# Kernel tuning notes

Measured on AMD Instinct MI355X. Metric: run time of the kernel, lower is better.

Reference implementation:

```python
import jax, jax.numpy as jnp
import numpy as np

NEG_INF = -1e10  # matches torch -10000000000.0


def setup_inputs() -> dict:
    key = jax.random.key(0)
    ks = jax.random.split(key, 8)
    L, B, E, H, HID, A = 2048, 32, 512, 512, 512, 512
    input_data = jax.random.normal(ks[0], (L, B, E), dtype=jnp.float32)
    mask = jax.random.randint(ks[1], (L, B), 0, 2, dtype=jnp.int32)
    action_feature = jax.random.normal(ks[2], (B, A), dtype=jnp.float32)
    hidden_state = jax.random.normal(ks[3], (B, H), dtype=jnp.float32)
    state = jax.random.normal(ks[4], (B, H), dtype=jnp.float32)
    W1 = jax.random.normal(ks[5], (H + E, HID), dtype=jnp.float32) * (1.0 / np.sqrt(H + E))
    b1 = jnp.zeros((HID,), dtype=jnp.float32)
    W2 = jax.random.normal(ks[6], (HID, 1), dtype=jnp.float32) * (1.0 / np.sqrt(HID))
    b2 = jnp.zeros((1,), dtype=jnp.float32)
    return {"input_data": input_data, "mask": mask, "action_feature": action_feature,
            "hidden_state": hidden_state, "state": state,
            "W1": W1, "b1": b1, "W2": W2, "b2": b2}


def reference(input_data, mask, action_feature, hidden_state, state, W1, b1, W2, b2):
    # input_data: (L, B, E); hidden_state: (B, H)
    H = hidden_state.shape[-1]
    # query = concat([hidden broadcast over L, input_data], -1); split W1 to avoid
    # materializing the (L, B, H+E) concat.
    W1_h, W1_e = W1[:H], W1[H:]                      # (H, HID), (E, HID)
    pre = hidden_state @ W1_h + b1                   # (B, HID)
    pre = pre[None] + jnp.einsum('lbe,eh->lbh', input_data, W1_e)  # (L, B, HID)
    logit = (jnp.tanh(pre) @ W2).squeeze(-1) + b2[0]  # (L, B)
    logit = jnp.where(mask != 0, logit, NEG_INF)
    p = jax.nn.softmax(logit, axis=0)                 # softmax over L
    ctx = jnp.einsum('lbe,lb->be', input_data, p)     # (B, E)
    return jnp.concatenate([ctx, action_feature], axis=1)
```

## Files before the change

### kernel.cpp

```cpp
#include <hip/hip_runtime.h>
#include <hip/hip_bf16.h>
#include <stdint.h>

#define L_DIM 2048
#define B_DIM 32
#define E_DIM 512
#define HID_DIM 512
#define M_DIM (L_DIM * B_DIM)

typedef float f32x4 __attribute__((ext_vector_type(4)));
typedef short bf16x8 __attribute__((ext_vector_type(8)));

#define OFF_BASE  0
#define OFF_WT    65536
#define OFF_LOGIT 589824
#define OFF_P     851968
#define OFF_PART  1114112

__device__ __forceinline__ unsigned short f2bf(float f) {
  unsigned int u = __float_as_uint(f);
  u = (u + 0x7FFFu + ((u >> 16) & 1u)) >> 16;
  return (unsigned short)u;
}

__device__ __forceinline__ float tanh_fast(float x) {
  float xc = fminf(fmaxf(x, -15.f), 15.f);
  float e = __expf(2.f * xc);
  return (e - 1.f) * __builtin_amdgcn_rcpf(e + 1.f);
}

__device__ __forceinline__ uint4 pack8(const float4& a, const float4& b) {
  uint4 r;
  r.x = (unsigned)f2bf(a.x) | ((unsigned)f2bf(a.y) << 16);
  r.y = (unsigned)f2bf(a.z) | ((unsigned)f2bf(a.w) << 16);
  r.z = (unsigned)f2bf(b.x) | ((unsigned)f2bf(b.y) << 16);
  r.w = (unsigned)f2bf(b.z) | ((unsigned)f2bf(b.w) << 16);
  return r;
}

__global__ __launch_bounds__(256) void k_base(const float* __restrict__ hidden,
                                              const float* __restrict__ W1,
                                              const float* __restrict__ b1,
                                              float* __restrict__ base) {
  const int b = blockIdx.x;
  const int tid = threadIdx.x;
  __shared__ float hs[HID_DIM];
  {
    float2 v = *(const float2*)(hidden + (size_t)b * 512 + tid * 2);
    hs[tid * 2] = v.x; hs[tid * 2 + 1] = v.y;
  }
  __syncthreads();
  const int h = tid * 2;
  float2 b1v = *(const float2*)(b1 + h);
  float ax = b1v.x, ay = b1v.y;
#pragma unroll 8
  for (int e = 0; e < 512; ++e) {
    float2 w = *(const float2*)(W1 + (size_t)e * 512 + h);
    float hv = hs[e];
    ax = fmaf(hv, w.x, ax);
    ay = fmaf(hv, w.y, ay);
  }
  float2 r; r.x = ax; r.y = ay;
  *(float2*)(base + (size_t)b * 512 + h) = r;
}

__global__ __launch_bounds__(256) void k_prep_wt(const float* __restrict__ W1,
                                                 unsigned short* __restrict__ Wt) {
  const int kc = blockIdx.x;
  const int tid = threadIdx.x;
  __shared__ unsigned short sh[32][520];
#pragma unroll
  for (int i = 0; i < 16; ++i) {
    int flat4 = i * 256 + tid;
    int r = flat4 >> 7;
    int c = (flat4 & 127) * 4;
    float4 v = *(const float4*)(W1 + (size_t)(512 + kc * 32 + r) * 512 + c);
    sh[r][c + 0] = f2bf(v.x); sh[r][c + 1] = f2bf(v.y);
    sh[r][c + 2] = f2bf(v.z); sh[r][c + 3] = f2bf(v.w);
  }
  __syncthreads();
#pragma unroll
  for (int j = 0; j < 2; ++j) {
    int n = tid * 2 + j;
    alignas(16) unsigned short ov[32];
#pragma unroll
    for (int kl = 0; kl < 32; ++kl) ov[kl] = sh[kl][n];
    uint4* dst = (uint4*)(Wt + ((size_t)kc * 16384 + (size_t)n * 32));
    const uint4* s = (const uint4*)ov;
    dst[0] = s[0]; dst[1] = s[1]; dst[2] = s[2]; dst[3] = s[3];
  }
}

__global__ __launch_bounds__(512, 2) void k_logits(
    const float* __restrict__ x, const unsigned short* __restrict__ Wt,
    const float* __restrict__ base, const float* __restrict__ W2,
    float* __restrict__ logit) {
  __shared__ unsigned short xs[2][128 * 32];
  __shared__ unsigned short wl[2][512 * 32];
  const int tid = threadIdx.x;
  const int m0 = blockIdx.x * 128;
  const int wid = tid >> 6, lane = tid & 63;
  const int wm = wid >> 2, wn = wid & 3;
  const int lg = lane >> 4, l15 = lane & 15;

  const int xr = tid >> 2;
  const int xk = (tid & 3) * 8;
  const float* xsrc = x + (size_t)(m0 + xr) * 512 + xk;

  {
    float4 a0 = *(const float4*)(xsrc + 0);
    float4 a1 = *(const float4*)(xsrc + 4);
    const uint4* s = (const uint4*)(Wt + (size_t)tid * 32);
    uint4 w0 = s[0], w1 = s[1], w2_ = s[2], w3 = s[3];
    *(uint4*)(&xs[0][xr * 32 + xk]) = pack8(a0, a1);
    uint4* wd = (uint4*)(&wl[0][tid * 32]);
    wd[(0 + tid) & 3] = w0; wd[(1 + tid) & 3] = w1;
    wd[(2 + tid) & 3] = w2_; wd[(3 + tid) & 3] = w3;
  }
  __syncthreads();

  f32x4 acc[4][8];
#pragma unroll
  for (int mi = 0; mi < 4; ++mi)
#pragma unroll
    for (int ni = 0; ni < 8; ++ni) acc[mi][ni] = (f32x4){0.f, 0.f, 0.f, 0.f};

  for (int kc = 0; kc < 16; ++kc) {
    const int cur = kc & 1;
    float4 nxa, nxb; uint4 nw0, nw1, nw2, nw3;
    if (kc < 15) {
      nxa = *(const float4*)(xsrc + (kc + 1) * 32);
      nxb = *(const float4*)(xsrc + (kc + 1) * 32 + 4);
      const uint4* s = (const uint4*)(Wt + (size_t)(kc + 1) * 16384 + (size_t)tid * 32);
      nw0 = s[0]; nw1 = s[1]; nw2 = s[2]; nw3 = s[3];
    }
    bf16x8 af[4];
#pragma unroll
    for (int mi = 0; mi < 4; ++mi) {
      int r = wm * 64 + mi * 16 + l15;
      af[mi] = *(const bf16x8*)(&xs[cur][r * 32 + lg * 8]);
    }
    bf16x8 bf[8];
#pragma unroll
    for (int ni = 0; ni < 8; ++ni) {
      int n = wn * 128 + ni * 16 + l15;
      bf[ni] = *(const bf16x8*)(&wl[cur][n * 32 + ((lg + n) & 3) * 8]);
    }
#pragma unroll
    for (int mi = 0; mi < 4; ++mi)
#pragma unroll
      for (int ni = 0; ni < 8; ++ni)
        acc[mi][ni] = __builtin_amdgcn_mfma_f32_16x16x32_bf16(af[mi], bf[ni], acc[mi][ni], 0, 0, 0);
    if (kc < 15) {
      const int nb = cur ^ 1;
      *(uint4*)(&xs[nb][xr * 32 + xk]) = pack8(nxa, nxb);
      uint4* wd = (uint4*)(&wl[nb][tid * 32]);
      wd[(0 + tid) & 3] = nw0; wd[(1 + tid) & 3] = nw1;
      wd[(2 + tid) & 3] = nw2; wd[(3 + tid) & 3] = nw3;
    }
    __syncthreads();
  }

  float w2v[8];
#pragma unroll
  for (int ni = 0; ni < 8; ++ni) w2v[ni] = W2[wn * 128 + ni * 16 + l15];
  float lsum[4][4];
#pragma unroll
  for (int mi = 0; mi < 4; ++mi) {
#pragma unroll
    for (int rg = 0; rg < 4; ++rg) {
      int m = m0 + wm * 64 + mi * 16 + lg * 4 + rg;
      int bb = m & 31;
      const float* brow = base + (size_t)bb * 512 + wn * 128;
      float s = 0.f;
#pragma unroll
      for (int ni = 0; ni < 8; ++ni) {
        float pre = acc[mi][ni][rg] + brow[ni * 16 + l15];
        s = fmaf(tanh_fast(pre), w2v[ni], s);
      }
      lsum[mi][rg] = s;
    }
  }
  float (*lred)[4][64] = (float (*)[4][64])xs;
#pragma unroll
  for (int mi = 0; mi < 4; ++mi)
#pragma unroll
    for (int rg = 0; rg < 4; ++rg) {
      float v = lsum[mi][rg];
      v += __shfl_xor(v, 1); v += __shfl_xor(v, 2);
      v += __shfl_xor(v, 4); v += __shfl_xor(v, 8);
      if (l15 == 0) lred[wm][wn][mi * 16 + lg * 4 + rg] = v;
    }
  __syncthreads();
  if (tid < 128) {
    const int wmr = tid >> 6, row = tid & 63;
    float v = (lred[wmr][0][row] + lred[wmr][1][row]) +
              (lred[wmr][2][row] + lred[wmr][3][row]);
    logit[m0 + tid] = v;
  }
}

__global__ __launch_bounds__(256) void k_softmax(const float* __restrict__ logit,
                                                 const int* __restrict__ mask,
                                                 float* __restrict__ p) {
  const int b = blockIdx.x, tid = threadIdx.x;
  float lv[8]; float mx = -3.0e38f;
#pragma unroll
  for (int i = 0; i < 8; ++i) {
    int idx = (tid + i * 256) * 32 + b;
    float v = (mask[idx] != 0) ? logit[idx] : -1.0e10f;
    lv[i] = v; mx = fmaxf(mx, v);
  }
  __shared__ float red[8];
  for (int d = 1; d < 64; d <<= 1) mx = fmaxf(mx, __shfl_xor(mx, d));
  if ((tid & 63) == 0) red[tid >> 6] = mx;
  __syncthreads();
  mx = fmaxf(fmaxf(red[0], red[1]), fmaxf(red[2], red[3]));
  float s = 0.f;
#pragma unroll
  for (int i = 0; i < 8; ++i) { lv[i] = __expf(lv[i] - mx); s += lv[i]; }
  for (int d = 1; d < 64; d <<= 1) s += __shfl_xor(s, d);
  __syncthreads();
  if ((tid & 63) == 0) red[4 + (tid >> 6)] = s;
  __syncthreads();
  s = (red[4] + red[5]) + (red[6] + red[7]);
  float inv = 1.f / s;
#pragma unroll
  for (int i = 0; i < 8; ++i) {
    int idx = (tid + i * 256) * 32 + b;
    p[idx] = lv[i] * inv;
  }
}

__global__ __launch_bounds__(256) void k_ctx(const float* __restrict__ x,
                                             const float* __restrict__ p,
                                             float* __restrict__ part) {
  const int blk = blockIdx.x;
  const int b = blk >> 5, ch = blk & 31;
  const int tid = threadIdx.x;
  __shared__ float ps[64];
  const int l0 = ch * 64;
  if (tid < 64) ps[tid] = p[(l0 + tid) * 32 + b];
  __syncthreads();
  const float* xb = x + ((size_t)l0 * 32 + b) * 512 + tid * 2;
  float ax = 0.f, ay = 0.f;
#pragma unroll 4
  for (int i = 0; i < 64; ++i) {
    float2 v = *(const float2*)(xb + (size_t)i * 32 * 512);
    float pv = ps[i];
    ax = fmaf(pv, v.x, ax); ay = fmaf(pv, v.y, ay);
  }
  float2 r; r.x = ax; r.y = ay;
  *(float2*)(part + (size_t)blk * 512 + tid * 2) = r;
}

__global__ __launch_bounds__(256) void k_final(const float* __restrict__ part,
                                               const float* __restrict__ af,
                                               float* __restrict__ out) {
  const int b = blockIdx.x, tid = threadIdx.x;
  float ax = 0.f, ay = 0.f;
#pragma unroll
  for (int ch = 0; ch < 32; ++ch) {
    float2 v = *(const float2*)(part + ((size_t)(b * 32 + ch) * 512) + tid * 2);
    ax += v.x; ay += v.y;
  }
  float2 r; r.x = ax; r.y = ay;
  *(float2*)(out + (size_t)b * 1024 + tid * 2) = r;
  float2 a = *(const float2*)(af + (size_t)b * 512 + tid * 2);
  *(float2*)(out + (size_t)b * 1024 + 512 + tid * 2) = a;
}

extern "C" void kernel_launch(void* const* d_in, const int* in_sizes, int n_in,
                              void* d_out, int out_size, void* d_ws, size_t ws_size,
                              hipStream_t stream) {
  const float* x      = (const float*)d_in[0];
  const int*   mask   = (const int*)d_in[1];
  const float* af     = (const float*)d_in[2];
  const float* hidden = (const float*)d_in[3];
  const float* W1     = (const float*)d_in[5];
  const float* b1     = (const float*)d_in[6];
  const float* W2     = (const float*)d_in[7];
  float* out = (float*)d_out;
  char* ws = (char*)d_ws;
  float*          base  = (float*)(ws + OFF_BASE);
  unsigned short* Wt    = (unsigned short*)(ws + OFF_WT);
  float*          logit = (float*)(ws + OFF_LOGIT);
  float*          p     = (float*)(ws + OFF_P);
  float*          part  = (float*)(ws + OFF_PART);

  k_base   <<<32,   256, 0, stream>>>(hidden, W1, b1, base);
  k_prep_wt<<<16,   256, 0, stream>>>(W1, Wt);
  k_logits <<<512,  512, 0, stream>>>(x, Wt, base, W2, logit);
  k_softmax<<<32,   256, 0, stream>>>(logit, mask, p);
  k_ctx    <<<1024, 256, 0, stream>>>(x, p, part);
  k_final  <<<32,   256, 0, stream>>>(part, af, out);
}
```

Measured before the change: 123.3 us.

## Pre-swizzle W1 and x tiles into MFMA fragment order; widen ctx loads

The weight prep kernel now writes W1 in the exact per-lane fragment order the MFMA loop consumes. The x tile is also stored to shared memory in fragment order, so each lane reads its operand with one contiguous 16-byte LDS load and neither bank swizzling nor strided row access is needed. Global weight loads become fully coalesced uint4 reads across threads instead of 64-byte runs per thread. Separately, the ctx reduction uses float4 loads with 128 threads per block instead of float2 with 256.

New measurement: 118.5 us. -3.8%, faster.

```diff
diff --git a/kernel.cpp b/kernel.cpp
--- a/kernel.cpp
+++ b/kernel.cpp
@@ -68,26 +68,26 @@
                                                  unsigned short* __restrict__ Wt) {
   const int kc = blockIdx.x;
   const int tid = threadIdx.x;
-  __shared__ unsigned short sh[32][520];
+  __shared__ unsigned short sh[32][516];
 #pragma unroll
   for (int i = 0; i < 16; ++i) {
-    int flat4 = i * 256 + tid;
-    int r = flat4 >> 7;
-    int c = (flat4 & 127) * 4;
+    int f4 = i * 256 + tid;
+    int r = f4 >> 7;
+    int c = (f4 & 127) * 4;
     float4 v = *(const float4*)(W1 + (size_t)(512 + kc * 32 + r) * 512 + c);
     sh[r][c + 0] = f2bf(v.x); sh[r][c + 1] = f2bf(v.y);
     sh[r][c + 2] = f2bf(v.z); sh[r][c + 3] = f2bf(v.w);
   }
   __syncthreads();
 #pragma unroll
-  for (int j = 0; j < 2; ++j) {
-    int n = tid * 2 + j;
-    alignas(16) unsigned short ov[32];
-#pragma unroll
-    for (int kl = 0; kl < 32; ++kl) ov[kl] = sh[kl][n];
-    uint4* dst = (uint4*)(Wt + ((size_t)kc * 16384 + (size_t)n * 32));
-    const uint4* s = (const uint4*)ov;
-    dst[0] = s[0]; dst[1] = s[1]; dst[2] = s[2]; dst[3] = s[3];
+  for (int i = 0; i < 8; ++i) {
+    int u = i * 256 + tid;
+    int n = ((u >> 9) << 7) + (((u >> 6) & 7) << 4) + (u & 15);
+    int k0 = ((u >> 4) & 3) << 3;
+    alignas(16) unsigned short tmp[8];
+#pragma unroll
+    for (int j = 0; j < 8; ++j) tmp[j] = sh[k0 + j][n];
+    *(uint4*)(Wt + ((size_t)kc * 2048 + u) * 8) = *(const uint4*)tmp;
   }
 }
 
@@ -95,8 +95,8 @@
     const float* __restrict__ x, const unsigned short* __restrict__ Wt,
     const float* __restrict__ base, const float* __restrict__ W2,
     float* __restrict__ logit) {
-  __shared__ unsigned short xs[2][128 * 32];
-  __shared__ unsigned short wl[2][512 * 32];
+  __shared__ unsigned short xs[2][4096];
+  __shared__ unsigned short wl[2][16384];
   const int tid = threadIdx.x;
   const int m0 = blockIdx.x * 128;
   const int wid = tid >> 6, lane = tid & 63;
@@ -104,18 +104,20 @@
   const int lg = lane >> 4, l15 = lane & 15;
 
   const int xr = tid >> 2;
-  const int xk = (tid & 3) * 8;
-  const float* xsrc = x + (size_t)(m0 + xr) * 512 + xk;
+  const int xks = tid & 3;
+  const float* xsrc = x + (size_t)(m0 + xr) * 512 + xks * 8;
+  const int xu = ((xr >> 4) << 6) + (xks << 4) + (xr & 15);
 
   {
     float4 a0 = *(const float4*)(xsrc + 0);
     float4 a1 = *(const float4*)(xsrc + 4);
-    const uint4* s = (const uint4*)(Wt + (size_t)tid * 32);
-    uint4 w0 = s[0], w1 = s[1], w2_ = s[2], w3 = s[3];
-    *(uint4*)(&xs[0][xr * 32 + xk]) = pack8(a0, a1);
-    uint4* wd = (uint4*)(&wl[0][tid * 32]);
-    wd[(0 + tid) & 3] = w0; wd[(1 + tid) & 3] = w1;
-    wd[(2 + tid) & 3] = w2_; wd[(3 + tid) & 3] = w3;
+    *(uint4*)(&xs[0][xu * 8]) = pack8(a0, a1);
+    const uint4* s = (const uint4*)Wt;
+#pragma unroll
+    for (int j = 0; j < 4; ++j) {
+      uint4 w = s[j * 512 + tid];
+      *(uint4*)(&wl[0][(j * 512 + tid) * 8]) = w;
+    }
   }
   __syncthreads();
 
@@ -127,36 +129,33 @@
 
   for (int kc = 0; kc < 16; ++kc) {
     const int cur = kc & 1;
-    float4 nxa, nxb; uint4 nw0, nw1, nw2, nw3;
+    float4 nxa, nxb; uint4 nw[4];
     if (kc < 15) {
       nxa = *(const float4*)(xsrc + (kc + 1) * 32);
       nxb = *(const float4*)(xsrc + (kc + 1) * 32 + 4);
-      const uint4* s = (const uint4*)(Wt + (size_t)(kc + 1) * 16384 + (size_t)tid * 32);
-      nw0 = s[0]; nw1 = s[1]; nw2 = s[2]; nw3 = s[3];
+      const uint4* s = (const uint4*)(Wt) + (size_t)(kc + 1) * 2048;
+#pragma unroll
+      for (int j = 0; j < 4; ++j) nw[j] = s[j * 512 + tid];
     }
     bf16x8 af[4];
 #pragma unroll
-    for (int mi = 0; mi < 4; ++mi) {
-      int r = wm * 64 + mi * 16 + l15;
-      af[mi] = *(const bf16x8*)(&xs[cur][r * 32 + lg * 8]);
-    }
-    bf16x8 bf[8];
-#pragma unroll
-    for (int ni = 0; ni < 8; ++ni) {
-      int n = wn * 128 + ni * 16 + l15;
-      bf[ni] = *(const bf16x8*)(&wl[cur][n * 32 + ((lg + n) & 3) * 8]);
-    }
-#pragma unroll
     for (int mi = 0; mi < 4; ++mi)
+      af[mi] = *(const bf16x8*)(&xs[cur][((wm * 4 + mi) * 64 + lane) * 8]);
+    bf16x8 bfv[8];
+#pragma unroll
+    for (int ni = 0; ni < 8; ++ni)
+      bfv[ni] = *(const bf16x8*)(&wl[cur][(wn * 512 + ni * 64 + lane) * 8]);
+#pragma unroll
+    for (int mi = 0; mi < 4; ++mi)
 #pragma unroll
       for (int ni = 0; ni < 8; ++ni)
-        acc[mi][ni] = __builtin_amdgcn_mfma_f32_16x16x32_bf16(af[mi], bf[ni], acc[mi][ni], 0, 0, 0);
+        acc[mi][ni] = __builtin_amdgcn_mfma_f32_16x16x32_bf16(af[mi], bfv[ni], acc[mi][ni], 0, 0, 0);
     if (kc < 15) {
       const int nb = cur ^ 1;
-      *(uint4*)(&xs[nb][xr * 32 + xk]) = pack8(nxa, nxb);
-      uint4* wd = (uint4*)(&wl[nb][tid * 32]);
-      wd[(0 + tid) & 3] = nw0; wd[(1 + tid) & 3] = nw1;
-      wd[(2 + tid) & 3] = nw2; wd[(3 + tid) & 3] = nw3;
+      *(uint4*)(&xs[nb][xu * 8]) = pack8(nxa, nxb);
+#pragma unroll
+      for (int j = 0; j < 4; ++j)
+        *(uint4*)(&wl[nb][(j * 512 + tid) * 8]) = nw[j];
     }
     __syncthreads();
   }
@@ -232,7 +231,7 @@
   }
 }
 
-__global__ __launch_bounds__(256) void k_ctx(const float* __restrict__ x,
+__global__ __launch_bounds__(128) void k_ctx(const float* __restrict__ x,
                                              const float* __restrict__ p,
                                              float* __restrict__ part) {
   const int blk = blockIdx.x;
@@ -242,16 +241,17 @@
   const int l0 = ch * 64;
   if (tid < 64) ps[tid] = p[(l0 + tid) * 32 + b];
   __syncthreads();
-  const float* xb = x + ((size_t)l0 * 32 + b) * 512 + tid * 2;
-  float ax = 0.f, ay = 0.f;
+  const float* xb = x + ((size_t)l0 * 32 + b) * 512 + tid * 4;
+  float ax = 0.f, ay = 0.f, az = 0.f, aw = 0.f;
 #pragma unroll 4
   for (int i = 0; i < 64; ++i) {
-    float2 v = *(const float2*)(xb + (size_t)i * 32 * 512);
+    float4 v = *(const float4*)(xb + (size_t)i * 32 * 512);
     float pv = ps[i];
     ax = fmaf(pv, v.x, ax); ay = fmaf(pv, v.y, ay);
-  }
-  float2 r; r.x = ax; r.y = ay;
-  *(float2*)(part + (size_t)blk * 512 + tid * 2) = r;
+    az = fmaf(pv, v.z, az); aw = fmaf(pv, v.w, aw);
+  }
+  float4 r; r.x = ax; r.y = ay; r.z = az; r.w = aw;
+  *(float4*)(part + (size_t)blk * 512 + tid * 4) = r;
 }
 
 __global__ __launch_bounds__(256) void k_final(const float* __restrict__ part,
@@ -292,6 +292,6 @@
   k_prep_wt<<<16,   256, 0, stream>>>(W1, Wt);
   k_logits <<<512,  512, 0, stream>>>(x, Wt, base, W2, logit);
   k_softmax<<<32,   256, 0, stream>>>(logit, mask, p);
-  k_ctx    <<<1024, 256, 0, stream>>>(x, p, part);
+  k_ctx    <<<1024, 128, 0, stream>>>(x, p, part);
   k_final  <<<32,   256, 0, stream>>>(part, af, out);
 }
```
